# Kernel optimization log

Hardware: AMD Instinct MI355X
Metric: run time of the kernel (lower is better)

## Reference

```python
import jax, jax.numpy as jnp
import numpy as np

EPS = 1e-5
NEG_SLOPE = 0.2
KMAX = 30
MS_LIST = (10, 20, 30)  # ms_list=[10,20] with kmax=30 appended, as in get_graph_feature


def _lrelu(h):
    return jnp.where(h > 0, h, NEG_SLOPE * h)


def _bn_eval(h, gamma, beta):
    # eval-mode BatchNorm2d with running_mean=0, running_var=1
    scale = gamma / jnp.sqrt(1.0 + EPS)
    return h * scale[None, :, None, None] + beta[None, :, None, None]


def setup_inputs() -> dict:
    key = jax.random.key(0)
    ks = jax.random.split(key, 5)
    B, C, N = 8, 3, 4096
    x = jax.random.normal(ks[0], (B, C, N), dtype=jnp.float32)
    w1 = jax.random.normal(ks[1], (64, 6), dtype=jnp.float32) * 0.2
    w2 = jax.random.normal(ks[2], (64, 64), dtype=jnp.float32) * 0.1
    wa = jax.random.normal(ks[3], (1, 64), dtype=jnp.float32) * 0.1
    return {
        "x": x,
        "w1": w1, "g1": jnp.ones((64,), jnp.float32), "b1": jnp.zeros((64,), jnp.float32),
        "w2": w2, "g2": jnp.ones((64,), jnp.float32), "b2": jnp.zeros((64,), jnp.float32),
        "wa": wa, "ba": jnp.zeros((1,), jnp.float32),
        "ga": jnp.ones((1,), jnp.float32), "bga": jnp.zeros((1,), jnp.float32),
    }


def _knn_idx(x, k):
    # x: [B, C, N]; pairwise_distance[b,i,j] = -||xi||^2 + 2 xi.xj - ||xj||^2
    xx = jnp.sum(x * x, axis=1, keepdims=True)            # [B, 1, N]
    inner = jnp.einsum('bcn,bcm->bnm', x, x)              # [B, N, N]
    pd = 2.0 * inner - xx - jnp.swapaxes(xx, 1, 2)        # [B, N, N]
    _, idx = jax.lax.top_k(pd, k)                         # [B, N, k], sorted nearest-first
    return idx


def reference(x, w1, g1, b1, w2, g2, b2, wa, ba, ga, bga):
    B, C, N = x.shape
    idx = _knn_idx(x, KMAX)                               # [B, N, KMAX]
    xt = jnp.transpose(x, (0, 2, 1))                      # [B, N, C]
    # one gather at kmax; per-scale feats are prefixes of the sorted neighbor list
    neigh = jax.vmap(lambda xb, ib: xb[ib])(xt, idx)      # [B, N, KMAX, C]

    acc = 0.0
    for k in MS_LIST:
        feat_k = neigh[:, :, :k, :]                       # [B, N, k, C]
        center = jnp.broadcast_to(xt[:, :, None, :], (B, N, k, C))
        f = jnp.concatenate([feat_k - center, center], axis=-1)   # [B, N, k, 2C]
        f = jnp.transpose(f, (0, 3, 1, 2))                # [B, 2C, N, k]

        h = _lrelu(_bn_eval(jnp.einsum('oi,bink->bonk', w1, f), g1, b1))
        h = _lrelu(_bn_eval(jnp.einsum('oi,bink->bonk', w2, h), g2, b2))
        a = jnp.einsum('oi,bink->bonk', wa, h) + ba[None, :, None, None]
        a = _lrelu(_bn_eval(a, ga, bga))                  # [B, 1, N, k]
        a = jax.nn.softmax(a, axis=-1)
        # attention-weighted neighbor pooling -> [B, 64, N]
        acc = acc + jnp.einsum('bnk,bcnk->bcn', a[:, 0], h)
    return acc / len(MS_LIST)
```

## Files before the change

kernel.cpp:

```cpp
#include <hip/hip_runtime.h>
#include <math.h>


#define NB 8
#define NPT 4096
#define KMAXK 30
#define ROWS (NB * NPT)
#define QW 8
#define SCAP 96

typedef __attribute__((ext_vector_type(8))) short short8v;
typedef __attribute__((ext_vector_type(4))) float float4v;

__device__ __forceinline__ unsigned long long shflx64(unsigned long long v, int m) {
  unsigned lo = (unsigned)__shfl_xor((int)(unsigned)(v & 0xFFFFFFFFull), m, 64);
  unsigned hi = (unsigned)__shfl_xor((int)(unsigned)(v >> 32), m, 64);
  return ((unsigned long long)hi << 32) | (unsigned long long)lo;
}

__device__ __forceinline__ short f2bf(float x) {
  unsigned u = __float_as_uint(x);
  return (short)((u + 0x7FFFu + ((u >> 16) & 1u)) >> 16);
}

__device__ __forceinline__ unsigned ordkey(float f) {
  const unsigned bits = __float_as_uint(f);
  return bits ^ ((unsigned)((int)bits >> 31) | 0x80000000u);
}

__device__ __forceinline__ float sbcast(float v) {
  return __int_as_float(__builtin_amdgcn_readfirstlane(__float_as_int(v)));
}

__global__ __launch_bounds__(256) void prep_kernel(const float* __restrict__ x,
                                                   const float* __restrict__ w2,
                                                   float4v* __restrict__ xq,
                                                   short8v* __restrict__ w2bf) {
  const int i = blockIdx.x * 256 + threadIdx.x;
  if (i < ROWS) {
    const int b = i >> 12, m = i & (NPT - 1);
    const float* xb = x + (size_t)b * 3 * NPT;
    const float y0 = xb[m], y1 = xb[NPT + m], y2 = xb[2 * NPT + m];
    const float xx = y0 * y0 + y1 * y1 + y2 * y2;
    xq[i] = (float4v){y0, y1, y2, xx};
  }
  if (blockIdx.x == ROWS / 256) {
#pragma unroll
    for (int u = 0; u < 2; ++u) {
      const int v = threadIdx.x * 2 + u;
      const int lane = v & 63, fi = v >> 6;
      const int kt = fi >> 2, nt = fi & 3;
      const int q = lane & 15, g = lane >> 4;
      const float* src = w2 + (nt * 16 + q) * 64 + kt * 32 + g * 8;
      short8v tt;
#pragma unroll
      for (int e = 0; e < 8; ++e) tt[e] = f2bf(src[e]);
      w2bf[v] = tt;
    }
  }
}

__global__ __launch_bounds__(256, 6) void knn_kernel(const float4v* __restrict__ xq,
                                                     int* __restrict__ knn) {
  __shared__ unsigned long long buf[4][QW][SCAP];
  const int wv = threadIdx.x >> 6;
  const int lane = threadIdx.x & 63;
  const int row0 = ((blockIdx.x << 2) + wv) * QW;
  const int b = row0 >> 12;
  const int n0 = row0 & (NPT - 1);
  const float4v* xqb = xq + ((size_t)b << 12);

  float qx[QW], qy[QW], qz[QW], qq[QW];
#pragma unroll
  for (int qi = 0; qi < QW; ++qi) {
    const float4v qv = xqb[n0 + qi];
    qx[qi] = sbcast(qv[0]);
    qy[qi] = sbcast(qv[1]);
    qz[qi] = sbcast(qv[2]);
    qq[qi] = sbcast(qv[3]);
  }

  float kmax[QW];
#pragma unroll
  for (int qi = 0; qi < QW; ++qi) kmax[qi] = -3.0e38f;
  for (int j = 0; j < 64; ++j) {
    const int m = (j << 6) + lane;
    const float4v c = xqb[m];
#pragma unroll
    for (int qi = 0; qi < QW; ++qi) {
      float inner = c[0] * qx[qi];
      inner = fmaf(c[1], qy[qi], inner);
      inner = fmaf(c[2], qz[qi], inner);
      const float pd = 2.0f * inner - qq[qi] - c[3];
      kmax[qi] = fmaxf(kmax[qi], pd);
    }
  }

  float thr[QW];
#pragma unroll
  for (int qi = 0; qi < QW; ++qi) {
    float v = kmax[qi];
#pragma unroll
    for (int kk = 2; kk <= 64; kk <<= 1) {
#pragma unroll
      for (int jj = 32; jj >= 1; jj >>= 1) {
        if (jj < kk) {
          const float o = __shfl_xor(v, jj, 64);
          const bool up = ((lane & kk) == 0);
          const bool takeMax = (((lane & jj) != 0) == up);
          v = takeMax ? fmaxf(v, o) : fminf(v, o);
        }
      }
    }
    thr[qi] = sbcast(__shfl(v, 34, 64));
  }

  int cnt[QW];
#pragma unroll
  for (int qi = 0; qi < QW; ++qi) cnt[qi] = 0;
  for (int j = 0; j < 64; ++j) {
    const int m = (j << 6) + lane;
    const float4v c = xqb[m];
#pragma unroll
    for (int qi = 0; qi < QW; ++qi) {
      float inner = c[0] * qx[qi];
      inner = fmaf(c[1], qy[qi], inner);
      inner = fmaf(c[2], qz[qi], inner);
      const float pd = 2.0f * inner - qq[qi] - c[3];
      const bool pred = pd >= thr[qi];
      const unsigned long long mask = __ballot(pred);
      if (pred) {
        const int pos = cnt[qi] + (int)__popcll(mask & ((1ull << lane) - 1ull));
        if (pos < SCAP) {
          buf[wv][qi][pos] = ((unsigned long long)ordkey(pd) << 32) | (unsigned)(4095 - m);
        }
      }
      cnt[qi] += (int)__popcll(mask);
    }
  }

#pragma unroll 1
  for (int qi = 0; qi < QW; ++qi) {
    const int c = cnt[qi];
    const int outbase = (row0 + qi) * 32;
    if (c >= KMAXK && c <= 64) {
      unsigned long long val = (lane < c) ? buf[wv][qi][lane] : 0ull;
#pragma unroll
      for (int kk = 2; kk <= 64; kk <<= 1) {
#pragma unroll
        for (int jj = 32; jj >= 1; jj >>= 1) {
          if (jj < kk) {
            const unsigned long long o = shflx64(val, jj);
            const bool up = ((lane & kk) == 0);
            const bool takeMax = (((lane & jj) != 0) == up);
            const unsigned long long mx = val > o ? val : o;
            const unsigned long long mn = val > o ? o : val;
            val = takeMax ? mx : mn;
          }
        }
      }
      const int rank = 63 - lane;
      if (rank < KMAXK) {
        const int m = 4095 - (int)(val & 0xFFFFFFFFull);
        knn[outbase + rank] = m;
      }
    } else if (c > 64 && c <= SCAP) {
      for (int r = 0; r < KMAXK; ++r) {
        unsigned long long lmax = 0ull;
        int lpos = -1;
        for (int p = lane; p < c; p += 64) {
          const unsigned long long q2 = buf[wv][qi][p];
          if (q2 > lmax) { lmax = q2; lpos = p; }
        }
        unsigned long long g = lmax;
#pragma unroll
        for (int s = 32; s >= 1; s >>= 1) {
          const unsigned long long o = shflx64(g, s);
          g = o > g ? o : g;
        }
        const unsigned long long pm = __ballot(lmax == g && lpos >= 0);
        const int lowlane = (int)(__ffsll((unsigned long long)pm) - 1);
        if (lane == lowlane) buf[wv][qi][lpos] = 0ull;
        if (lane == 0) knn[outbase + r] = 4095 - (int)(g & 0xFFFFFFFFull);
      }
    } else {
      unsigned long long prev = ~0ull;
      for (int r = 0; r < KMAXK; ++r) {
        unsigned long long best = 0ull;
        for (int j = 0; j < 64; ++j) {
          const int m = (j << 6) + lane;
          const float4v cc = xqb[m];
          float inner = cc[0] * qx[qi];
          inner = fmaf(cc[1], qy[qi], inner);
          inner = fmaf(cc[2], qz[qi], inner);
          const float pd = 2.0f * inner - qq[qi] - cc[3];
          const unsigned long long key =
              ((unsigned long long)ordkey(pd) << 32) | (unsigned)(4095 - m);
          if (key < prev && key > best) best = key;
        }
#pragma unroll
        for (int s = 32; s >= 1; s >>= 1) {
          const unsigned long long o = shflx64(best, s);
          best = o > best ? o : best;
        }
        if (lane == 0) knn[outbase + r] = 4095 - (int)(best & 0xFFFFFFFFull);
        prev = best;
      }
    }
  }
}

__global__ __launch_bounds__(256) void pcc_mlp_mfma(
    const float4v* __restrict__ xq, const float* __restrict__ w1,
    const float* __restrict__ g1, const float* __restrict__ b1,
    const short8v* __restrict__ w2bf, const float* __restrict__ g2,
    const float* __restrict__ b2, const float* __restrict__ wa,
    const float* __restrict__ ba, const float* __restrict__ ga,
    const float* __restrict__ bga, const int* __restrict__ knn,
    float* __restrict__ out) {
  __shared__ float w1row[64][8];
  const int tid = threadIdx.x;
  const float invs = 1.0f / sqrtf(1.0f + 1e-5f);
  for (int idx = tid; idx < 512; idx += 256) {
    const int c = idx >> 3, s = idx & 7;
    float v;
    if (s < 6) v = w1[c * 6 + s];
    else if (s == 6) v = g1[c] * invs;
    else v = b1[c];
    w1row[c][s] = v;
  }
  __syncthreads();

  const int wv = tid >> 6, lane = tid & 63;
  const int q = lane & 15, g = lane >> 4;
  const int row = (blockIdx.x << 2) + wv;
  const int b = row >> 12, n = row & (NPT - 1);
  const float4v* xqb = xq + ((size_t)b << 12);

  short8v bf[2][4];
#pragma unroll
  for (int kt = 0; kt < 2; ++kt)
#pragma unroll
    for (int nt = 0; nt < 4; ++nt) bf[kt][nt] = w2bf[((kt << 2) + nt) * 64 + lane];

  float s2r[4], be2r[4], war[4];
#pragma unroll
  for (int nt = 0; nt < 4; ++nt) {
    s2r[nt] = g2[q + 16 * nt] * invs;
    be2r[nt] = b2[q + 16 * nt];
    war[nt] = wa[q + 16 * nt];
  }
  const float sa = ga[0] * invs, ba0 = ba[0], bga0 = bga[0];

  const float4v qv = xqb[n];
  const float xn0 = qv[0], xn1 = qv[1], xn2 = qv[2];

  const int j0 = knn[row * 32 + q];
  const float4v c0 = xqb[j0];
  float a1x = xn0, a1y = xn1, a1z = xn2;
  if (q < 14) {
    const int j1 = knn[row * 32 + 16 + q];
    const float4v c1 = xqb[j1];
    a1x = c1[0]; a1y = c1[1]; a1z = c1[2];
  }
  const float d0x = c0[0] - xn0, d0y = c0[1] - xn1, d0z = c0[2] - xn2;
  const float d1x = a1x - xn0, d1y = a1y - xn1, d1z = a1z - xn2;

  float4v dfr[2][4];
#pragma unroll
  for (int mt = 0; mt < 2; ++mt)
#pragma unroll
    for (int nt = 0; nt < 4; ++nt) dfr[mt][nt] = (float4v){0.f, 0.f, 0.f, 0.f};

#pragma unroll
  for (int kt = 0; kt < 2; ++kt) {
    short8v af0, af1;
#pragma unroll
    for (int e = 0; e < 8; ++e) {
      const int c = kt * 32 + g * 8 + e;
      const float4v wlo = *(const float4v*)&w1row[c][0];
      const float4v whi = *(const float4v*)&w1row[c][4];
      float h = wlo[0] * d0x;
      h = fmaf(wlo[1], d0y, h);
      h = fmaf(wlo[2], d0z, h);
      h = fmaf(wlo[3], xn0, h);
      h = fmaf(whi[0], xn1, h);
      h = fmaf(whi[1], xn2, h);
      h = fmaf(h, whi[2], whi[3]);
      h = fmaxf(h, 0.2f * h);
      af0[e] = f2bf(h);
      float h1v = wlo[0] * d1x;
      h1v = fmaf(wlo[1], d1y, h1v);
      h1v = fmaf(wlo[2], d1z, h1v);
      h1v = fmaf(wlo[3], xn0, h1v);
      h1v = fmaf(whi[0], xn1, h1v);
      h1v = fmaf(whi[1], xn2, h1v);
      h1v = fmaf(h1v, whi[2], whi[3]);
      h1v = fmaxf(h1v, 0.2f * h1v);
      af1[e] = f2bf(h1v);
    }
#pragma unroll
    for (int nt = 0; nt < 4; ++nt) {
      dfr[0][nt] = __builtin_amdgcn_mfma_f32_16x16x32_bf16(af0, bf[kt][nt], dfr[0][nt], 0, 0, 0);
      dfr[1][nt] = __builtin_amdgcn_mfma_f32_16x16x32_bf16(af1, bf[kt][nt], dfr[1][nt], 0, 0, 0);
    }
  }

  float part[2][4];
#pragma unroll
  for (int mt = 0; mt < 2; ++mt)
#pragma unroll
    for (int r = 0; r < 4; ++r) part[mt][r] = 0.f;
#pragma unroll
  for (int mt = 0; mt < 2; ++mt)
#pragma unroll
    for (int nt = 0; nt < 4; ++nt) {
      float4v d = dfr[mt][nt];
#pragma unroll
      for (int r = 0; r < 4; ++r) {
        float h2 = fmaf(d[r], s2r[nt], be2r[nt]);
        h2 = fmaxf(h2, 0.2f * h2);
        d[r] = h2;
        part[mt][r] = fmaf(war[nt], h2, part[mt][r]);
      }
      dfr[mt][nt] = d;
    }
#pragma unroll
  for (int mt = 0; mt < 2; ++mt)
#pragma unroll
    for (int r = 0; r < 4; ++r) {
      float p = part[mt][r];
      p += __shfl_xor(p, 1, 64);
      p += __shfl_xor(p, 2, 64);
      p += __shfl_xor(p, 4, 64);
      p += __shfl_xor(p, 8, 64);
      part[mt][r] = p;
    }

  const int mrow = g * 4;
  float sc0[4], sc1[4];
  float mloc = -3.0e38f;
#pragma unroll
  for (int r = 0; r < 4; ++r) {
    float a = fmaf(part[0][r] + ba0, sa, bga0);
    a = fmaxf(a, 0.2f * a);
    sc0[r] = a;
    mloc = fmaxf(mloc, a);
  }
#pragma unroll
  for (int r = 0; r < 4; ++r) {
    float a = fmaf(part[1][r] + ba0, sa, bga0);
    a = fmaxf(a, 0.2f * a);
    sc1[r] = a;
    if (mrow + r < 14) mloc = fmaxf(mloc, a);
  }
  mloc = fmaxf(mloc, __shfl_xor(mloc, 16, 64));
  mloc = fmaxf(mloc, __shfl_xor(mloc, 32, 64));

  float e0[4], e1[4];
  float l10 = 0.f, l20 = 0.f, l30 = 0.f;
#pragma unroll
  for (int r = 0; r < 4; ++r) {
    const float vv = expf(sc0[r] - mloc);
    e0[r] = vv;
    l30 += vv;
    l20 += vv;
    if (mrow + r < 10) l10 += vv;
  }
#pragma unroll
  for (int r = 0; r < 4; ++r) {
    const float vv = (mrow + r < 14) ? expf(sc1[r] - mloc) : 0.f;
    e1[r] = vv;
    l30 += vv;
    if (mrow + r < 4) l20 += vv;
  }
  l10 += __shfl_xor(l10, 16, 64); l10 += __shfl_xor(l10, 32, 64);
  l20 += __shfl_xor(l20, 16, 64); l20 += __shfl_xor(l20, 32, 64);
  l30 += __shfl_xor(l30, 16, 64); l30 += __shfl_xor(l30, 32, 64);
  const float i10 = 1.0f / l10, i20 = 1.0f / l20, i30 = 1.0f / l30;
  const float third = 1.0f / 3.0f;

  float wgt0[4], wgt1[4];
#pragma unroll
  for (int r = 0; r < 4; ++r) {
    wgt0[r] = e0[r] * (((mrow + r < 10) ? i10 : 0.f) + i20 + i30) * third;
    wgt1[r] = e1[r] * (((mrow + r < 4) ? i20 : 0.f) + i30) * third;
  }

  float acc[4] = {0.f, 0.f, 0.f, 0.f};
#pragma unroll
  for (int nt = 0; nt < 4; ++nt) {
#pragma unroll
    for (int r = 0; r < 4; ++r) {
      acc[nt] = fmaf(wgt0[r], dfr[0][nt][r], acc[nt]);
      acc[nt] = fmaf(wgt1[r], dfr[1][nt][r], acc[nt]);
    }
  }
#pragma unroll
  for (int nt = 0; nt < 4; ++nt) {
    acc[nt] += __shfl_xor(acc[nt], 16, 64);
    acc[nt] += __shfl_xor(acc[nt], 32, 64);
  }
  const float val = (g == 0) ? acc[0] : (g == 1) ? acc[1] : (g == 2) ? acc[2] : acc[3];
  out[(size_t)(b * 64 + q + 16 * g) * NPT + n] = val;
}

extern "C" void kernel_launch(void* const* d_in, const int* in_sizes, int n_in,
                              void* d_out, int out_size, void* d_ws, size_t ws_size,
                              hipStream_t stream) {
  const float* x = (const float*)d_in[0];
  const float* w1 = (const float*)d_in[1];
  const float* g1 = (const float*)d_in[2];
  const float* b1 = (const float*)d_in[3];
  const float* w2 = (const float*)d_in[4];
  const float* g2 = (const float*)d_in[5];
  const float* b2 = (const float*)d_in[6];
  const float* wa = (const float*)d_in[7];
  const float* ba = (const float*)d_in[8];
  const float* ga = (const float*)d_in[9];
  const float* bga = (const float*)d_in[10];
  float* out = (float*)d_out;

  float4v* xq = (float4v*)d_ws;
  int* knn = (int*)((char*)d_ws + ROWS * 16);
  short8v* w2bf = (short8v*)((char*)d_ws + ROWS * 16 + ROWS * 32 * 4);

  prep_kernel<<<dim3(ROWS / 256 + 1), dim3(256), 0, stream>>>(x, w2, xq, w2bf);
  knn_kernel<<<dim3(ROWS / (4 * QW)), dim3(256), 0, stream>>>(xq, knn);
  pcc_mlp_mfma<<<dim3(ROWS / 4), dim3(256), 0, stream>>>(
      xq, w1, g1, b1, w2bf, g2, b2, wa, ba, ga, bga, knn, out);
}
```

Before: 149.9 us.

## Halve queries per wave and vectorize kNN distance math with packed float2

Reduces queries per wavefront from 8 to 4, which doubles the number of waves scanning candidates. It also rewrites the distance and max computations using float2 vectors so the compiler can emit packed FP32 instructions. The selection threshold is lowered by a small epsilon, which lets more candidates through and tolerates rounding differences between the two distance passes. In exchange, each candidate point is reloaded by more waves, and the shared buffer per block shrinks with QW.

```diff
diff --git a/kernel.cpp b/kernel.cpp
--- a/kernel.cpp
+++ b/kernel.cpp
@@ -6,11 +6,12 @@
 #define NPT 4096
 #define KMAXK 30
 #define ROWS (NB * NPT)
-#define QW 8
+#define QW 4
 #define SCAP 96
 
 typedef __attribute__((ext_vector_type(8))) short short8v;
 typedef __attribute__((ext_vector_type(4))) float float4v;
+typedef __attribute__((ext_vector_type(2))) float float2v;
 
 __device__ __forceinline__ unsigned long long shflx64(unsigned long long v, int m) {
   unsigned lo = (unsigned)__shfl_xor((int)(unsigned)(v & 0xFFFFFFFFull), m, 64);
@@ -79,27 +80,39 @@
     qz[qi] = sbcast(qv[2]);
     qq[qi] = sbcast(qv[3]);
   }
-
-  float kmax[QW];
-#pragma unroll
-  for (int qi = 0; qi < QW; ++qi) kmax[qi] = -3.0e38f;
+  float2v qxp[2], qyp[2], qzp[2], qqp[2];
+#pragma unroll
+  for (int p = 0; p < 2; ++p) {
+    qxp[p] = (float2v){qx[2 * p], qx[2 * p + 1]};
+    qyp[p] = (float2v){qy[2 * p], qy[2 * p + 1]};
+    qzp[p] = (float2v){qz[2 * p], qz[2 * p + 1]};
+    qqp[p] = (float2v){qq[2 * p], qq[2 * p + 1]};
+  }
+
+  float2v kmaxp[2];
+  kmaxp[0] = (float2v){-3.0e38f, -3.0e38f};
+  kmaxp[1] = (float2v){-3.0e38f, -3.0e38f};
   for (int j = 0; j < 64; ++j) {
-    const int m = (j << 6) + lane;
-    const float4v c = xqb[m];
-#pragma unroll
-    for (int qi = 0; qi < QW; ++qi) {
-      float inner = c[0] * qx[qi];
-      inner = fmaf(c[1], qy[qi], inner);
-      inner = fmaf(c[2], qz[qi], inner);
-      const float pd = 2.0f * inner - qq[qi] - c[3];
-      kmax[qi] = fmaxf(kmax[qi], pd);
-    }
-  }
+    const float4v c = xqb[(j << 6) + lane];
+    const float2v cx = (float2v){c[0], c[0]};
+    const float2v cy = (float2v){c[1], c[1]};
+    const float2v cz = (float2v){c[2], c[2]};
+    const float2v cw = (float2v){c[3], c[3]};
+#pragma unroll
+    for (int p = 0; p < 2; ++p) {
+      float2v inner = cx * qxp[p];
+      inner = __builtin_elementwise_fma(cy, qyp[p], inner);
+      inner = __builtin_elementwise_fma(cz, qzp[p], inner);
+      const float2v pd = (inner + inner) - qqp[p] - cw;
+      kmaxp[p] = __builtin_elementwise_max(kmaxp[p], pd);
+    }
+  }
+  const float kmaxs[QW] = {kmaxp[0][0], kmaxp[0][1], kmaxp[1][0], kmaxp[1][1]};
 
   float thr[QW];
 #pragma unroll
   for (int qi = 0; qi < QW; ++qi) {
-    float v = kmax[qi];
+    float v = kmaxs[qi];
 #pragma unroll
     for (int kk = 2; kk <= 64; kk <<= 1) {
 #pragma unroll
@@ -112,7 +125,7 @@
         }
       }
     }
-    thr[qi] = sbcast(__shfl(v, 34, 64));
+    thr[qi] = sbcast(__shfl(v, 34, 64)) - 1.0e-4f;
   }
 
   int cnt[QW];
@@ -121,12 +134,21 @@
   for (int j = 0; j < 64; ++j) {
     const int m = (j << 6) + lane;
     const float4v c = xqb[m];
+    const float2v cx = (float2v){c[0], c[0]};
+    const float2v cy = (float2v){c[1], c[1]};
+    const float2v cz = (float2v){c[2], c[2]};
+    const float2v cw = (float2v){c[3], c[3]};
+    float2v pdp[2];
+#pragma unroll
+    for (int p = 0; p < 2; ++p) {
+      float2v inner = cx * qxp[p];
+      inner = __builtin_elementwise_fma(cy, qyp[p], inner);
+      inner = __builtin_elementwise_fma(cz, qzp[p], inner);
+      pdp[p] = (inner + inner) - qqp[p] - cw;
+    }
 #pragma unroll
     for (int qi = 0; qi < QW; ++qi) {
-      float inner = c[0] * qx[qi];
-      inner = fmaf(c[1], qy[qi], inner);
-      inner = fmaf(c[2], qz[qi], inner);
-      const float pd = 2.0f * inner - qq[qi] - c[3];
+      const float pd = pdp[qi >> 1][qi & 1];
       const bool pred = pd >= thr[qi];
       const unsigned long long mask = __ballot(pred);
       if (pred) {
```

Measured after the change: 146.8 us. 1.02x faster.
